# Kernel tuning notes

Hardware: AMD Instinct MI355X
Metric: run time of the kernel (lower is better)

Reference implementation:

```python
import jax, jax.numpy as jnp
import numpy as np

B, C, T, H, W, E, K = 2, 256, 16, 32, 32, 4, 2


def setup_inputs() -> dict:
    key = jax.random.key(0)
    ks = jax.random.split(key, 5)
    x = jax.random.normal(ks[0], (B, C, T, H, W), dtype=jnp.float32)
    # gate: Conv3d(dim, E, 1) -> weight [E, C], bias [E]
    gate_w = jax.random.normal(ks[1], (E, C), dtype=jnp.float32) * 0.02
    gate_b = jnp.zeros((E,), dtype=jnp.float32)
    # experts_layer1: Conv3d(dim, dim*E, 1) -> weight [E*C, C], bias [E*C]
    w1 = jax.random.normal(ks[2], (E * C, C), dtype=jnp.float32) * 0.02
    b1 = jnp.zeros((E * C,), dtype=jnp.float32)
    # experts_layer2: Conv3d(dim*E, dim*E, 1, groups=E) -> per-expert [C, C]
    w2 = jax.random.normal(ks[3], (E, C, C), dtype=jnp.float32) * 0.02
    b2 = jnp.zeros((E, C), dtype=jnp.float32)
    return {"x": x, "gate_w": gate_w, "gate_b": gate_b,
            "w1": w1, "b1": b1, "w2": w2, "b2": b2}


def reference(x, gate_w, gate_b, w1, b1, w2, b2):
    # gating: 1x1x1 conv == channel contraction; logits [B,T,H,W,E]
    logits = jnp.einsum('bcthw,ec->bthwe', x, gate_w) + gate_b
    vals, idx = jax.lax.top_k(logits, K)              # [B,T,H,W,K]
    wk = jax.nn.softmax(vals, axis=-1).astype(x.dtype)
    # scatter top-k softmax weights back into E slots (zeros elsewhere)
    weights = jnp.sum(jax.nn.one_hot(idx, E, dtype=x.dtype) * wk[..., None],
                      axis=-2)                        # [B,T,H,W,E]
    # layer1 (dense 1x1x1 conv) + SiLU; output channels = E*C
    h = jax.nn.silu(jnp.einsum('bcthw,oc->bothw', x, w1)
                    + b1[None, :, None, None, None])
    h = h.reshape(B, E, C, T, H, W)
    # layer2: grouped 1x1x1 conv, one [C,C] matmul per expert
    expert_out = (jnp.einsum('becthw,eoc->beothw', h, w2)
                  + b2[None, :, :, None, None, None])  # [B,E,C,T,H,W]
    # weighted combine over experts + residual
    out = jnp.einsum('becthw,bthwe->bcthw', expert_out, weights)
    return out + x
```

## Files before the change

kernel.cpp:

```cpp
#include <hip/hip_runtime.h>
#include <hip/hip_bf16.h>


#define C_DIM 256
#define S_DIM 16384
#define E_DIM 4
#define MT 128
#define XST 264
#define WFRAG_ELEMS 262144

typedef __attribute__((ext_vector_type(8))) short bf16x8;
typedef __attribute__((ext_vector_type(4))) float f32x4;

__device__ __forceinline__ short bfq(float f) {
  __hip_bfloat16 h = __float2bfloat16(f);
  return *(short*)&h;
}

__global__ __launch_bounds__(256) void prepack_kernel(
    const float* __restrict__ w1, const float* __restrict__ w2,
    __hip_bfloat16* __restrict__ dst)
{
  int o8   = blockIdx.x * 256 + threadIdx.x;
  int half = o8 >> 15;
  int idx  = o8 & 32767;
  int j    = idx & 31;
  int rowid= idx >> 5;
  int e    = rowid >> 8;
  int nt   = (rowid >> 4) & 15;
  int row  = rowid & 15;
  int kc   = j >> 2;
  int col8 = j & 3;
  int lane = (col8 << 4) | row;
  const float* src = half ? w2 : w1;
  const float* s = src + rowid * 256 + j * 8;
  const float4 v0 = *(const float4*)s;
  const float4 v1 = *(const float4*)(s + 4);
  bf16x8 outv = {bfq(v0.x), bfq(v0.y), bfq(v0.z), bfq(v0.w),
                 bfq(v1.x), bfq(v1.y), bfq(v1.z), bfq(v1.w)};
  int chunk = ((e*16 + nt)*8 + kc)*64 + lane;
  *(bf16x8*)((short*)dst + half*WFRAG_ELEMS + chunk*8) = outv;
}

template<int MTC>
__device__ __forceinline__ void gemm1_sparse(
    const short* XsS, short* HsS, const short* w1e, const float* b1e,
    const unsigned char* plist_e, const float* wgtg_e,
    int nv, int r, int q, bool dosync)
{
  f32x4 hacc[MTC][2];
#pragma unroll
  for (int i = 0; i < MTC; ++i)
#pragma unroll
    for (int j = 0; j < 2; ++j) hacc[i][j] = (f32x4){0.f, 0.f, 0.f, 0.f};

  int aoff[MTC];
#pragma unroll
  for (int Mt = 0; Mt < MTC; ++Mt)
    aoff[Mt] = (int)plist_e[Mt*16 + r] * XST;

  bf16x8 bw[2][2];
#pragma unroll
  for (int t = 0; t < 2; ++t) bw[0][t] = *(const bf16x8*)(w1e + (t*8 + 0)*512);
#pragma unroll
  for (int kc = 0; kc < 8; ++kc) {
    if (kc < 7) {
#pragma unroll
      for (int t = 0; t < 2; ++t)
        bw[(kc+1)&1][t] = *(const bf16x8*)(w1e + (t*8 + kc + 1)*512);
    }
    bf16x8 a[MTC];
#pragma unroll
    for (int Mt = 0; Mt < MTC; ++Mt)
      a[Mt] = *(const bf16x8*)(XsS + aoff[Mt] + kc*32 + q*8);
#pragma unroll
    for (int Mt = 0; Mt < MTC; ++Mt)
#pragma unroll
      for (int t = 0; t < 2; ++t)
        hacc[Mt][t] = __builtin_amdgcn_mfma_f32_16x16x32_bf16(a[Mt], bw[kc&1][t], hacc[Mt][t], 0, 0, 0);
  }

  if (dosync) __syncthreads();

#pragma unroll
  for (int Mt = 0; Mt < MTC; ++Mt) {
    const int g0 = Mt*16 + q*4;
    const unsigned pw = *(const unsigned*)(plist_e + g0);
    const f32x4 wg = *(const f32x4*)(wgtg_e + g0);
#pragma unroll
    for (int t = 0; t < 2; ++t) {
      const int n = nv*32 + t*16 + r;
      const float bias = b1e[n];
#pragma unroll
      for (int reg = 0; reg < 4; ++reg) {
        const int p = (pw >> (8*reg)) & 255;
        const float z = hacc[Mt][t][reg] + bias;
        const float s = __builtin_amdgcn_rcpf(1.0f + __expf(-z));
        HsS[p*XST + n] = bfq(z * s * wg[reg]);
      }
    }
  }
}

__global__ __launch_bounds__(1024, 4) void moe_fused_kernel(
    const float* __restrict__ x,
    const float* __restrict__ gate_w,
    const float* __restrict__ gate_b,
    const float* __restrict__ b1,
    const float* __restrict__ b2,
    const __hip_bfloat16* __restrict__ wp,
    float* __restrict__ out)
{
  __shared__ __align__(16) char pool[2 * MT * XST * 2];
  __shared__ __align__(16) float Wgt[MT * 4];
  __shared__ __align__(16) unsigned char plist[4][192];
  __shared__ __align__(16) float WgtG[4][192];
  __shared__ __align__(4)  unsigned char zlist[4][128];
  __shared__ int mcnt[4];

  short* XsS = (short*)pool;
  short* HsS = (short*)(pool + MT * XST * 2);

  const int tid  = threadIdx.x;
  const int lane = tid & 63;
  const int wv   = tid >> 6;
  const int nv   = wv & 7;
  const int mh   = wv >> 3;
  const int r    = lane & 15;
  const int q    = lane >> 4;

  const int g  = blockIdx.x;
  const int b  = g >> 7;
  const int s0 = (g & 127) * MT;
  const float* xb = x + (size_t)b * C_DIM * S_DIM + s0;

  const short* W1P = (const short*)wp;
  const short* W2P = (const short*)wp + WFRAG_ELEMS;

  {
    const int p  = mh*64 + lane;
    const int c0 = nv * 32;
    float xv[32];
#pragma unroll
    for (int j = 0; j < 32; ++j)
      xv[j] = xb[(size_t)(c0 + j) * S_DIM + p];

    double acc[4] = {0.0, 0.0, 0.0, 0.0};
#pragma unroll
    for (int j = 0; j < 32; ++j) {
      const double xd = (double)xv[j];
      acc[0] += xd * (double)gate_w[0*256 + c0 + j];
      acc[1] += xd * (double)gate_w[1*256 + c0 + j];
      acc[2] += xd * (double)gate_w[2*256 + c0 + j];
      acc[3] += xd * (double)gate_w[3*256 + c0 + j];
    }

#pragma unroll
    for (int k = 0; k < 4; ++k) {
      bf16x8 blk = {bfq(xv[k*8+0]), bfq(xv[k*8+1]), bfq(xv[k*8+2]), bfq(xv[k*8+3]),
                    bfq(xv[k*8+4]), bfq(xv[k*8+5]), bfq(xv[k*8+6]), bfq(xv[k*8+7])};
      *(bf16x8*)(XsS + p*XST + c0 + k*8) = blk;
    }

    double* GateD = (double*)HsS;
#pragma unroll
    for (int e = 0; e < 4; ++e)
      GateD[(e*8 + nv)*128 + p] = acc[e];
  }
  __syncthreads();

  if (tid < 512) {
    const int p = tid >> 2;
    const int e = tid & 3;
    const double* GateD = (const double*)HsS;
    double s = (double)gate_b[e];
#pragma unroll
    for (int g2 = 0; g2 < 8; ++g2) s += GateD[(e*8 + g2)*128 + p];
    const float la = (float)s;
    const float lb = __shfl_xor(la, 1, 64);
    const float lc = __shfl_xor(la, 2, 64);
    const float ld = __shfl_xor(lb, 2, 64);
    if (e == 0) {
      const float l0 = la, l1 = lb, l2 = lc, l3 = ld;
      int i1 = 0; float v1 = l0;
      if (l1 > v1) { v1 = l1; i1 = 1; }
      if (l2 > v1) { v1 = l2; i1 = 2; }
      if (l3 > v1) { v1 = l3; i1 = 3; }
      float v2 = -3.0e38f; int i2 = 0;
      if (i1 != 0 && l0 > v2) { v2 = l0; i2 = 0; }
      if (i1 != 1 && l1 > v2) { v2 = l1; i2 = 1; }
      if (i1 != 2 && l2 > v2) { v2 = l2; i2 = 2; }
      if (i1 != 3 && l3 > v2) { v2 = l3; i2 = 3; }
      const float wA = 1.0f / (1.0f + __expf(v2 - v1));
      const float wB = 1.0f - wA;
      f32x4 w;
      w[0] = (i1 == 0) ? wA : ((i2 == 0) ? wB : 0.0f);
      w[1] = (i1 == 1) ? wA : ((i2 == 1) ? wB : 0.0f);
      w[2] = (i1 == 2) ? wA : ((i2 == 2) ? wB : 0.0f);
      w[3] = (i1 == 3) ? wA : ((i2 == 3) ? wB : 0.0f);
      *(f32x4*)(&Wgt[p*4]) = w;
    }
  }
  __syncthreads();

  if (wv < 4) {
    const int e = wv;
    int base = 0, zbase = 0;
#pragma unroll
    for (int half = 0; half < 2; ++half) {
      const int p = half*64 + lane;
      const float w = Wgt[p*4 + e];
      const bool sel = (w != 0.0f);
      const unsigned long long mask = __ballot(sel);
      const int below = __popcll(mask & ((1ull << lane) - 1ull));
      const int m = __popcll(mask);
      if (sel) {
        plist[e][base + below] = (unsigned char)p;
        WgtG[e][base + below]  = w;
      } else {
        zlist[e][zbase + lane - below] = (unsigned char)p;
      }
      base += m; zbase += 64 - m;
    }
    const int me  = base;
    const int mt2 = (me + 31) >> 5;
    const int pad = mt2*32 - me;
    if (lane < pad) {
      plist[e][me + lane] = zlist[e][lane];
      WgtG[e][me + lane]  = 0.0f;
    }
    if (lane == 0) mcnt[e] = me;
  }
  __syncthreads();

  f32x4 oacc[4][2];
#pragma unroll
  for (int i = 0; i < 4; ++i)
#pragma unroll
    for (int j = 0; j < 2; ++j) oacc[i][j] = (f32x4){0.f, 0.f, 0.f, 0.f};

  for (int e = 0; e < E_DIM; ++e) {
    const int me  = mcnt[e];
    const int mt2 = __builtin_amdgcn_readfirstlane((me + 31) >> 5);
    const short* w1e = W1P + ((e*16 + nv*2)*8)*512 + lane*8;
    const float* b1e = b1 + e*256;
    const unsigned char* pl = plist[e] + mh*mt2*16;
    const float*         wg = WgtG[e]  + mh*mt2*16;
    const bool dosync = (e > 0);

    if      (mt2 == 2) gemm1_sparse<2>(XsS, HsS, w1e, b1e, pl, wg, nv, r, q, dosync);
    else if (mt2 == 1) gemm1_sparse<1>(XsS, HsS, w1e, b1e, pl, wg, nv, r, q, dosync);
    else if (mt2 == 3) gemm1_sparse<3>(XsS, HsS, w1e, b1e, pl, wg, nv, r, q, dosync);
    else if (mt2 == 4) gemm1_sparse<4>(XsS, HsS, w1e, b1e, pl, wg, nv, r, q, dosync);
    else { if (dosync) __syncthreads(); }

    const short* w2e = W2P + ((e*16 + nv*2)*8)*512 + lane*8;
    bf16x8 cw[2][2];
#pragma unroll
    for (int t = 0; t < 2; ++t) cw[0][t] = *(const bf16x8*)(w2e + (t*8 + 0)*512);

    {
      const int zm = MT - me;
      const bf16x8 zz = {0,0,0,0,0,0,0,0};
      for (int i = tid; i < zm*32; i += 1024) {
        const int row = zlist[e][i >> 5];
        *(bf16x8*)(HsS + row*XST + (i & 31)*8) = zz;
      }
    }
    __syncthreads();

    {
#pragma unroll
      for (int kc = 0; kc < 8; ++kc) {
        if (kc < 7) {
#pragma unroll
          for (int t = 0; t < 2; ++t)
            cw[(kc+1)&1][t] = *(const bf16x8*)(w2e + (t*8 + kc + 1)*512);
        }
        bf16x8 a[4];
#pragma unroll
        for (int Mt = 0; Mt < 4; ++Mt)
          a[Mt] = *(const bf16x8*)(HsS + (mh*64 + Mt*16 + r)*XST + kc*32 + q*8);
#pragma unroll
        for (int Mt = 0; Mt < 4; ++Mt)
#pragma unroll
          for (int t = 0; t < 2; ++t)
            oacc[Mt][t] = __builtin_amdgcn_mfma_f32_16x16x32_bf16(a[Mt], cw[kc&1][t], oacc[Mt][t], 0, 0, 0);
      }
    }
  }

  {
    float b2v[2][4];
#pragma unroll
    for (int t = 0; t < 2; ++t) {
      const int c = nv*32 + t*16 + r;
#pragma unroll
      for (int e = 0; e < 4; ++e) b2v[t][e] = b2[e*256 + c];
    }
    float* ob = out + (size_t)b * C_DIM * S_DIM + s0;
#pragma unroll
    for (int Mt = 0; Mt < 4; ++Mt) {
      const int pb = mh*64 + Mt*16 + q*4;
      f32x4 wv4[4];
#pragma unroll
      for (int reg = 0; reg < 4; ++reg)
        wv4[reg] = *(const f32x4*)(&Wgt[(pb + reg)*4]);
#pragma unroll
      for (int t = 0; t < 2; ++t) {
        const int c = nv*32 + t*16 + r;
        f32x4 v = oacc[Mt][t];
#pragma unroll
        for (int reg = 0; reg < 4; ++reg)
          v[reg] += wv4[reg][0]*b2v[t][0] + wv4[reg][1]*b2v[t][1]
                  + wv4[reg][2]*b2v[t][2] + wv4[reg][3]*b2v[t][3];
        const float4 xr = *(const float4*)(xb + (size_t)c*S_DIM + pb);
        float4 res;
        res.x = v[0] + xr.x; res.y = v[1] + xr.y;
        res.z = v[2] + xr.z; res.w = v[3] + xr.w;
        *(float4*)(ob + (size_t)c*S_DIM + pb) = res;
      }
    }
  }
}

extern "C" void kernel_launch(void* const* d_in, const int* in_sizes, int n_in,
                              void* d_out, int out_size, void* d_ws, size_t ws_size,
                              hipStream_t stream)
{
  (void)in_sizes; (void)n_in; (void)out_size; (void)ws_size;
  const float* x      = (const float*)d_in[0];
  const float* gate_w = (const float*)d_in[1];
  const float* gate_b = (const float*)d_in[2];
  const float* w1     = (const float*)d_in[3];
  const float* b1     = (const float*)d_in[4];
  const float* w2     = (const float*)d_in[5];
  const float* b2     = (const float*)d_in[6];
  float* out = (float*)d_out;
  __hip_bfloat16* wpack = (__hip_bfloat16*)d_ws;

  prepack_kernel<<<256, 256, 0, stream>>>(w1, w2, wpack);
  moe_fused_kernel<<<256, 1024, 0, stream>>>(x, gate_w, gate_b, b1, b2, wpack, out);
}
```

Measured before the change: 131.1 us.

## Retile MFMA wave grid to 4x4 with 64-column tiles and 16-row sparse padding

Changes the wave layout from 8 column-groups x 2 row-halves to 4 column-groups x 4 row-quarters, so each wave computes 64 output columns over 32 rows. Sparse GEMM1 tiles are now padded to multiples of 16 rows instead of 32 and interleaved across the four row-waves. The aim is less wasted MFMA work on padding rows and more weight-fragment reuse per A load. The cost is more B-fragment registers per wave and a possibly uneven split of GEMM1 work across waves.

```diff
diff --git a/kernel.cpp b/kernel.cpp
--- a/kernel.cpp
+++ b/kernel.cpp
@@ -42,59 +42,59 @@
   *(bf16x8*)((short*)dst + half*WFRAG_ELEMS + chunk*8) = outv;
 }
 
-template<int MTC>
+template<int TW>
 __device__ __forceinline__ void gemm1_sparse(
     const short* XsS, short* HsS, const short* w1e, const float* b1e,
     const unsigned char* plist_e, const float* wgtg_e,
-    int nv, int r, int q, bool dosync)
+    int mh, int nv, int r, int q, bool dosync)
 {
-  f32x4 hacc[MTC][2];
-#pragma unroll
-  for (int i = 0; i < MTC; ++i)
-#pragma unroll
-    for (int j = 0; j < 2; ++j) hacc[i][j] = (f32x4){0.f, 0.f, 0.f, 0.f};
-
-  int aoff[MTC];
-#pragma unroll
-  for (int Mt = 0; Mt < MTC; ++Mt)
-    aoff[Mt] = (int)plist_e[Mt*16 + r] * XST;
-
-  bf16x8 bw[2][2];
-#pragma unroll
-  for (int t = 0; t < 2; ++t) bw[0][t] = *(const bf16x8*)(w1e + (t*8 + 0)*512);
+  f32x4 hacc[TW][4];
+#pragma unroll
+  for (int i = 0; i < TW; ++i)
+#pragma unroll
+    for (int t = 0; t < 4; ++t) hacc[i][t] = (f32x4){0.f, 0.f, 0.f, 0.f};
+
+  int aoff[TW];
+#pragma unroll
+  for (int i = 0; i < TW; ++i)
+    aoff[i] = (int)plist_e[(mh + 4*i)*16 + r] * XST;
+
+  bf16x8 bw[2][4];
+#pragma unroll
+  for (int t = 0; t < 4; ++t) bw[0][t] = *(const bf16x8*)(w1e + (t*8 + 0)*512);
 #pragma unroll
   for (int kc = 0; kc < 8; ++kc) {
     if (kc < 7) {
 #pragma unroll
-      for (int t = 0; t < 2; ++t)
+      for (int t = 0; t < 4; ++t)
         bw[(kc+1)&1][t] = *(const bf16x8*)(w1e + (t*8 + kc + 1)*512);
     }
-    bf16x8 a[MTC];
-#pragma unroll
-    for (int Mt = 0; Mt < MTC; ++Mt)
-      a[Mt] = *(const bf16x8*)(XsS + aoff[Mt] + kc*32 + q*8);
-#pragma unroll
-    for (int Mt = 0; Mt < MTC; ++Mt)
-#pragma unroll
-      for (int t = 0; t < 2; ++t)
-        hacc[Mt][t] = __builtin_amdgcn_mfma_f32_16x16x32_bf16(a[Mt], bw[kc&1][t], hacc[Mt][t], 0, 0, 0);
+    bf16x8 a[TW];
+#pragma unroll
+    for (int i = 0; i < TW; ++i)
+      a[i] = *(const bf16x8*)(XsS + aoff[i] + kc*32 + q*8);
+#pragma unroll
+    for (int i = 0; i < TW; ++i)
+#pragma unroll
+      for (int t = 0; t < 4; ++t)
+        hacc[i][t] = __builtin_amdgcn_mfma_f32_16x16x32_bf16(a[i], bw[kc&1][t], hacc[i][t], 0, 0, 0);
   }
 
   if (dosync) __syncthreads();
 
 #pragma unroll
-  for (int Mt = 0; Mt < MTC; ++Mt) {
-    const int g0 = Mt*16 + q*4;
+  for (int i = 0; i < TW; ++i) {
+    const int g0 = (mh + 4*i)*16 + q*4;
     const unsigned pw = *(const unsigned*)(plist_e + g0);
     const f32x4 wg = *(const f32x4*)(wgtg_e + g0);
 #pragma unroll
-    for (int t = 0; t < 2; ++t) {
-      const int n = nv*32 + t*16 + r;
+    for (int t = 0; t < 4; ++t) {
+      const int n = nv*64 + t*16 + r;
       const float bias = b1e[n];
 #pragma unroll
       for (int reg = 0; reg < 4; ++reg) {
         const int p = (pw >> (8*reg)) & 255;
-        const float z = hacc[Mt][t][reg] + bias;
+        const float z = hacc[i][t][reg] + bias;
         const float s = __builtin_amdgcn_rcpf(1.0f + __expf(-z));
         HsS[p*XST + n] = bfq(z * s * wg[reg]);
       }
@@ -124,8 +124,8 @@
   const int tid  = threadIdx.x;
   const int lane = tid & 63;
   const int wv   = tid >> 6;
-  const int nv   = wv & 7;
-  const int mh   = wv >> 3;
+  const int nv   = wv & 3;
+  const int mh   = wv >> 2;
   const int r    = lane & 15;
   const int q    = lane >> 4;
 
@@ -138,8 +138,10 @@
   const short* W2P = (const short*)wp + WFRAG_ELEMS;
 
   {
-    const int p  = mh*64 + lane;
-    const int c0 = nv * 32;
+    const int sc = wv & 7;
+    const int sh = wv >> 3;
+    const int p  = sh*64 + lane;
+    const int c0 = sc * 32;
     float xv[32];
 #pragma unroll
     for (int j = 0; j < 32; ++j)
@@ -165,7 +167,7 @@
     double* GateD = (double*)HsS;
 #pragma unroll
     for (int e = 0; e < 4; ++e)
-      GateD[(e*8 + nv)*128 + p] = acc[e];
+      GateD[(e*8 + sc)*128 + p] = acc[e];
   }
   __syncthreads();
 
@@ -223,8 +225,8 @@
       base += m; zbase += 64 - m;
     }
     const int me  = base;
-    const int mt2 = (me + 31) >> 5;
-    const int pad = mt2*32 - me;
+    const int mt2 = (me + 15) >> 4;
+    const int pad = mt2*16 - me;
     if (lane < pad) {
       plist[e][me + lane] = zlist[e][lane];
       WgtG[e][me + lane]  = 0.0f;
@@ -233,31 +235,28 @@
   }
   __syncthreads();
 
-  f32x4 oacc[4][2];
-#pragma unroll
-  for (int i = 0; i < 4; ++i)
-#pragma unroll
-    for (int j = 0; j < 2; ++j) oacc[i][j] = (f32x4){0.f, 0.f, 0.f, 0.f};
+  f32x4 oacc[2][4];
+#pragma unroll
+  for (int i = 0; i < 2; ++i)
+#pragma unroll
+    for (int t = 0; t < 4; ++t) oacc[i][t] = (f32x4){0.f, 0.f, 0.f, 0.f};
 
   for (int e = 0; e < E_DIM; ++e) {
     const int me  = mcnt[e];
-    const int mt2 = __builtin_amdgcn_readfirstlane((me + 31) >> 5);
-    const short* w1e = W1P + ((e*16 + nv*2)*8)*512 + lane*8;
+    const int mt2 = __builtin_amdgcn_readfirstlane((me + 15) >> 4);
+    const short* w1e = W1P + ((e*16 + nv*4)*8)*512 + lane*8;
     const float* b1e = b1 + e*256;
-    const unsigned char* pl = plist[e] + mh*mt2*16;
-    const float*         wg = WgtG[e]  + mh*mt2*16;
     const bool dosync = (e > 0);
-
-    if      (mt2 == 2) gemm1_sparse<2>(XsS, HsS, w1e, b1e, pl, wg, nv, r, q, dosync);
-    else if (mt2 == 1) gemm1_sparse<1>(XsS, HsS, w1e, b1e, pl, wg, nv, r, q, dosync);
-    else if (mt2 == 3) gemm1_sparse<3>(XsS, HsS, w1e, b1e, pl, wg, nv, r, q, dosync);
-    else if (mt2 == 4) gemm1_sparse<4>(XsS, HsS, w1e, b1e, pl, wg, nv, r, q, dosync);
+    const int tw = (mt2 > mh) ? ((mt2 - mh + 3) >> 2) : 0;
+
+    if      (tw == 1) gemm1_sparse<1>(XsS, HsS, w1e, b1e, plist[e], WgtG[e], mh, nv, r, q, dosync);
+    else if (tw == 2) gemm1_sparse<2>(XsS, HsS, w1e, b1e, plist[e], WgtG[e], mh, nv, r, q, dosync);
     else { if (dosync) __syncthreads(); }
 
-    const short* w2e = W2P + ((e*16 + nv*2)*8)*512 + lane*8;
-    bf16x8 cw[2][2];
-#pragma unroll
-    for (int t = 0; t < 2; ++t) cw[0][t] = *(const bf16x8*)(w2e + (t*8 + 0)*512);
+    const short* w2e = W2P + ((e*16 + nv*4)*8)*512 + lane*8;
+    bf16x8 cw[2][4];
+#pragma unroll
+    for (int t = 0; t < 4; ++t) cw[0][t] = *(const bf16x8*)(w2e + (t*8 + 0)*512);
 
     {
       const int zm = MT - me;
@@ -274,42 +273,42 @@
       for (int kc = 0; kc < 8; ++kc) {
         if (kc < 7) {
 #pragma unroll
-          for (int t = 0; t < 2; ++t)
+          for (int t = 0; t < 4; ++t)
             cw[(kc+1)&1][t] = *(const bf16x8*)(w2e + (t*8 + kc + 1)*512);
         }
-        bf16x8 a[4];
-#pragma unroll
-        for (int Mt = 0; Mt < 4; ++Mt)
-          a[Mt] = *(const bf16x8*)(HsS + (mh*64 + Mt*16 + r)*XST + kc*32 + q*8);
-#pragma unroll
-        for (int Mt = 0; Mt < 4; ++Mt)
-#pragma unroll
-          for (int t = 0; t < 2; ++t)
-            oacc[Mt][t] = __builtin_amdgcn_mfma_f32_16x16x32_bf16(a[Mt], cw[kc&1][t], oacc[Mt][t], 0, 0, 0);
+        bf16x8 a[2];
+#pragma unroll
+        for (int Mtq = 0; Mtq < 2; ++Mtq)
+          a[Mtq] = *(const bf16x8*)(HsS + (mh*32 + Mtq*16 + r)*XST + kc*32 + q*8);
+#pragma unroll
+        for (int Mtq = 0; Mtq < 2; ++Mtq)
+#pragma unroll
+          for (int t = 0; t < 4; ++t)
+            oacc[Mtq][t] = __builtin_amdgcn_mfma_f32_16x16x32_bf16(a[Mtq], cw[kc&1][t], oacc[Mtq][t], 0, 0, 0);
       }
     }
   }
 
   {
-    float b2v[2][4];
-#pragma unroll
-    for (int t = 0; t < 2; ++t) {
-      const int c = nv*32 + t*16 + r;
+    float b2v[4][4];
+#pragma unroll
+    for (int t = 0; t < 4; ++t) {
+      const int c = nv*64 + t*16 + r;
 #pragma unroll
       for (int e = 0; e < 4; ++e) b2v[t][e] = b2[e*256 + c];
     }
     float* ob = out + (size_t)b * C_DIM * S_DIM + s0;
 #pragma unroll
-    for (int Mt = 0; Mt < 4; ++Mt) {
-      const int pb = mh*64 + Mt*16 + q*4;
+    for (int Mtq = 0; Mtq < 2; ++Mtq) {
+      const int pb = mh*32 + Mtq*16 + q*4;
       f32x4 wv4[4];
 #pragma unroll
       for (int reg = 0; reg < 4; ++reg)
         wv4[reg] = *(const f32x4*)(&Wgt[(pb + reg)*4]);
 #pragma unroll
-      for (int t = 0; t < 2; ++t) {
-        const int c = nv*32 + t*16 + r;
-        f32x4 v = oacc[Mt][t];
+      for (int t = 0; t < 4; ++t) {
+        const int c = nv*64 + t*16 + r;
+        f32x4 v = oacc[Mtq][t];
 #pragma unroll
         for (int reg = 0; reg < 4; ++reg)
           v[reg] += wv4[reg][0]*b2v[t][0] + wv4[reg][1]*b2v[t][1]
```

Measured after the change: 146.7 us. 1.12x slower.
